# Kernel tuning notes

Measured on AMD Instinct MI355X. Metric: run time of the kernel, lower is better.

The kernel has to match this reference:

```python
import jax, jax.numpy as jnp
import numpy as np

N_NODES = 50000
N_EDGES = 800000
F_IN = 128
HIDDEN = 128
N_CLASSES = 10
N_GRAPHS = 256


def _glorot(key, shape):
    lim = float(np.sqrt(6.0 / (shape[0] + shape[1])))
    return jax.random.uniform(key, shape, jnp.float32, -lim, lim)


def setup_inputs() -> dict:
    key = jax.random.key(0)
    ks = jax.random.split(key, 12)
    x = jax.random.normal(ks[0], (N_NODES, F_IN), jnp.float32)
    edge_index = jax.random.randint(ks[1], (2, N_EDGES), 0, N_NODES, jnp.int64)
    batch = jnp.sort(jax.random.randint(ks[2], (N_NODES,), 0, N_GRAPHS, jnp.int64))
    dims = [(F_IN, HIDDEN), (HIDDEN, HIDDEN), (HIDDEN, N_CLASSES)]
    params = {}
    for i, (din, dout) in enumerate(dims, start=1):
        params[f"Wl{i}"] = _glorot(ks[2 + 2 * i], (din, dout))   # lin_l: applied to aggregated neighbors (has bias)
        params[f"bl{i}"] = jnp.zeros((dout,), jnp.float32)
        params[f"Wr{i}"] = _glorot(ks[3 + 2 * i], (din, dout))   # lin_r: applied to root/self features (no bias)
    return {"x": x, "edge_index": edge_index, "batch": batch, **params}


def _sage_conv(x, src, dst, Wl, bl, Wr):
    # mean aggregation of source features at destination nodes
    msg = x[src]                                                    # [E, D] gather
    ssum = jax.ops.segment_sum(msg, dst, num_segments=N_NODES)      # [N, D]
    cnt = jax.ops.segment_sum(jnp.ones((src.shape[0],), x.dtype), dst, num_segments=N_NODES)
    agg = ssum / jnp.maximum(cnt, 1.0)[:, None]
    return agg @ Wl + bl + x @ Wr


def reference(x, edge_index, batch, Wl1, bl1, Wr1, Wl2, bl2, Wr2, Wl3, bl3, Wr3):
    src, dst = edge_index[0], edge_index[1]
    h = _sage_conv(x, src, dst, Wl1, bl1, Wr1)
    h = _sage_conv(h, src, dst, Wl2, bl2, Wr2)
    h = _sage_conv(h, src, dst, Wl3, bl3, Wr3)                      # [N, C]
    # global mean pool over graphs
    gsum = jax.ops.segment_sum(h, batch, num_segments=N_GRAPHS)     # [G, C]
    gcnt = jax.ops.segment_sum(jnp.ones((h.shape[0],), h.dtype), batch, num_segments=N_GRAPHS)
    pooled = gsum / jnp.maximum(gcnt, 1.0)[:, None]
    return jax.nn.log_softmax(pooled, axis=-1)
```

## Files before the change

kernel.cpp:

```cpp
#include <hip/hip_runtime.h>


#define CAP 48
#define EB 4096

typedef __attribute__((ext_vector_type(8))) short short8;
typedef __attribute__((ext_vector_type(4))) float floatx4;

static __device__ __forceinline__ unsigned short f2bf(float f) {
    unsigned int u = __float_as_uint(f);
    u += 0x7FFFu + ((u >> 16) & 1u);
    return (unsigned short)(u >> 16);
}
static __device__ __forceinline__ float bf2f(unsigned short b) {
    return __uint_as_float(((unsigned int)b) << 16);
}

__global__ void prep_weights(const float* __restrict__ Wl2, const float* __restrict__ Wr2,
                             const float* __restrict__ Wl3, const float* __restrict__ Wr3,
                             float* __restrict__ m2Mg,
                             int* __restrict__ zero_base, int zero_words,
                             unsigned int* __restrict__ mmz, unsigned int* __restrict__ zb32,
                             unsigned int* __restrict__ t3b32, int N,
                             const int* __restrict__ ei, int E, int ablk, int nbk,
                             unsigned int* __restrict__ bedges, int* __restrict__ runCnt) {
    __shared__ int hist[512];
    __shared__ float wtT_s[128 * 20];
    if (blockIdx.x < (unsigned)ablk) {
        for (int i = threadIdx.x; i < nbk; i += 256) hist[i] = 0;
        __syncthreads();
        int e0 = blockIdx.x * EB + threadIdx.x;
        unsigned int pk[16];
        int bk[16], loc[16];
#pragma unroll
        for (int k = 0; k < 16; ++k) {
            int e = e0 + k * 256;
            if (e < E) {
                int src = ei[e];
                int dst = ei[E + e];
                bk[k] = dst >> 7;
                pk[k] = ((unsigned int)(dst & 127) << 16) | (unsigned int)src;
                loc[k] = atomicAdd(&hist[bk[k]], 1);
            } else bk[k] = -1;
        }
        __syncthreads();
        for (int i = threadIdx.x; i < nbk; i += 256)
            runCnt[(size_t)blockIdx.x * nbk + i] = hist[i];
#pragma unroll
        for (int k = 0; k < 16; ++k)
            if (bk[k] >= 0 && loc[k] < CAP)
                bedges[((size_t)bk[k] * ablk + blockIdx.x) * CAP + loc[k]] = pk[k];
        return;
    }
    int rb = blockIdx.x - ablk;
    if (rb < 4) {
        const int tid = threadIdx.x;
        for (int i = tid; i < 2560; i += 256) {
            int f = i / 20, c = i - f * 20;
            wtT_s[i] = (c < 10) ? Wl3[f * 10 + c] : Wr3[f * 10 + (c - 10)];
        }
        __syncthreads();
        int jl = tid >> 3;
        int cg = tid & 7;
        int j = rb * 32 + jl;
        const float* w2row = ((cg < 4) ? Wl2 : Wr2) + (size_t)j * 128;
        int c20 = (cg & 3) * 5;
        float acc[5] = {0.f, 0.f, 0.f, 0.f, 0.f};
        for (int f4 = 0; f4 < 32; ++f4) {
            float4 wv = *(const float4*)&w2row[f4 * 4];
#pragma unroll
            for (int e = 0; e < 4; ++e) {
                float w = (e == 0) ? wv.x : (e == 1) ? wv.y : (e == 2) ? wv.z : wv.w;
                const float* wt = &wtT_s[(f4 * 4 + e) * 20 + c20];
#pragma unroll
                for (int i = 0; i < 5; ++i) acc[i] += w * wt[i];
            }
        }
        int cc = (cg >> 2) * 20 + c20;
#pragma unroll
        for (int i = 0; i < 5; ++i) m2Mg[j * 40 + cc + i] = acc[i];
        return;
    }
    if (rb == 4) {
        if (threadIdx.x < 10) mmz[(size_t)N * 10 + threadIdx.x] = 0;
        if (threadIdx.x >= 32 && threadIdx.x < 42)
            zb32[(size_t)N * 10 + (threadIdx.x - 32)] = 0;
        if (threadIdx.x >= 64 && threadIdx.x < 74)
            t3b32[(size_t)N * 10 + (threadIdx.x - 64)] = 0;
        return;
    }
    int i = (rb - 5) * 256 + threadIdx.x;
    if (i < zero_words) zero_base[i] = 0;
}

__global__ __launch_bounds__(256) void prep2(
    const float* __restrict__ Wl1, const float* __restrict__ Wr1,
    const float* __restrict__ Wl3, const float* __restrict__ Wr3,
    const float* __restrict__ bl1, const float* __restrict__ bl2,
    const float* __restrict__ m2Mg, short* __restrict__ Wq,
    float* __restrict__ cbv) {
    __shared__ float m2s[128 * 40];
    __shared__ float cL[32][20];
    const int tid = threadIdx.x;
    if (blockIdx.x == 4) {
        for (int i = tid; i < 512; i += 256) {
            int k = i >> 2, f = 60 + (i & 3);
            int ks = k >> 5, rem = k & 31, qq = rem >> 3, jj = rem & 7;
            int mi = f >> 4, m = f & 15, l = qq * 16 + m;
            Wq[(((mi * 4 + ks) * 64) + l) * 8 + jj] = 0;
        }
        if (tid < 40) {
            float s = 0.f;
            if (tid < 20) {
                for (int k = 0; k < 128; ++k) s += bl1[k] * m2Mg[k * 40 + tid];
            } else {
                int c = tid - 20;
                for (int k = 0; k < 128; ++k) s += bl1[k] * m2Mg[k * 40 + 20 + c];
                for (int f = 0; f < 128; ++f) {
                    float wt = (c < 10) ? Wl3[f * 10 + c] : Wr3[f * 10 + (c - 10)];
                    s += bl2[f] * wt;
                }
            }
            cbv[tid] = s;
        }
        return;
    }
    for (int i = tid; i < 5120; i += 256) m2s[i] = m2Mg[i];
    __syncthreads();
    int kl = tid >> 3;
    int cg = tid & 7;
    int k = blockIdx.x * 32 + kl;
    int c0 = (cg & 3) * 5;
    bool left = (cg < 4);
    const float* wrow = (left ? Wl1 : Wr1) + (size_t)k * 128;
    float accM[5] = {0.f, 0.f, 0.f, 0.f, 0.f};
    float accR[5] = {0.f, 0.f, 0.f, 0.f, 0.f};
    for (int j4 = 0; j4 < 32; ++j4) {
        float4 wv = *(const float4*)&wrow[j4 * 4];
#pragma unroll
        for (int e = 0; e < 4; ++e) {
            float w = (e == 0) ? wv.x : (e == 1) ? wv.y : (e == 2) ? wv.z : wv.w;
            const float* mr = &m2s[(j4 * 4 + e) * 40];
#pragma unroll
            for (int i = 0; i < 5; ++i) {
                accM[i] += w * mr[c0 + i];
                accR[i] += w * mr[20 + c0 + i];
            }
        }
    }
    if (left) {
#pragma unroll
        for (int i = 0; i < 5; ++i) cL[kl][c0 + i] = accR[i];
    }
    __syncthreads();
    int ks = k >> 5, rem = k & 31, qq = rem >> 3, jj = rem & 7;
#pragma unroll
    for (int i = 0; i < 5; ++i) {
        if (left) {
            int f = c0 + i;
            int mi = f >> 4, m = f & 15, l = qq * 16 + m;
            Wq[(((mi * 4 + ks) * 64) + l) * 8 + jj] = (short)f2bf(accM[i]);
        } else {
            int f = 20 + c0 + i;
            int mi = f >> 4, m = f & 15, l = qq * 16 + m;
            Wq[(((mi * 4 + ks) * 64) + l) * 8 + jj] =
                (short)f2bf(accM[i] + cL[kl][c0 + i]);
            int f2 = 40 + c0 + i;
            int mi2 = f2 >> 4, m2 = f2 & 15, l2 = qq * 16 + m2;
            Wq[(((mi2 * 4 + ks) * 64) + l2) * 8 + jj] = (short)f2bf(accR[i]);
        }
    }
}

__global__ __launch_bounds__(256) void fillX(
    const float* __restrict__ x, const short* __restrict__ Wq,
    const float* __restrict__ cbv, unsigned short* __restrict__ mm,
    float* __restrict__ bmrow, int N, int nbk, int ablk,
    const unsigned int* __restrict__ bedges, const int* __restrict__ runCnt,
    int* __restrict__ cnt, unsigned short* __restrict__ colbuf) {
    __shared__ unsigned short As[64 * 136];
    __shared__ int lcnt[128];
    if (blockIdx.x >= (unsigned)nbk) {
        int blk = blockIdx.x - nbk;
        int node0 = blk * 64;
#pragma unroll
        for (int c = 0; c < 8; ++c) {
            int idx = c * 256 + threadIdx.x;
            int r = idx >> 5;
            int c4 = idx & 31;
            int row = node0 + r;
            float4 v = make_float4(0.f, 0.f, 0.f, 0.f);
            if (row < N) v = *(const float4*)&x[(size_t)row * 128 + c4 * 4];
            ushort4 p;
            p.x = f2bf(v.x); p.y = f2bf(v.y); p.z = f2bf(v.z); p.w = f2bf(v.w);
            *(ushort4*)&As[r * 136 + c4 * 4] = p;
        }
        __syncthreads();

        const int w = threadIdx.x >> 6;
        const int lane = threadIdx.x & 63;
        const int q = lane >> 4;
        const int m = lane & 15;

        floatx4 acc[4] = {};
#pragma unroll
        for (int s = 0; s < 4; ++s) {
            short8 bfrag = *(const short8*)&As[(w * 16 + m) * 136 + s * 32 + q * 8];
#pragma unroll
            for (int mi = 0; mi < 4; ++mi) {
                short8 wf = *(const short8*)&Wq[((mi * 4 + s) * 64 + lane) * 8];
                acc[mi] = __builtin_amdgcn_mfma_f32_16x16x32_bf16(
                    wf, bfrag, acc[mi], 0, 0, 0);
            }
        }
        int node = node0 + w * 16 + m;
        if (node < N) {
#pragma unroll
            for (int mi = 0; mi < 4; ++mi) {
                int f0 = mi * 16 + q * 4;
                floatx4 a = acc[mi];
                if (f0 < 20) {
                    ushort4 p;
                    p.x = f2bf(a[0]); p.y = f2bf(a[1]);
                    p.z = f2bf(a[2]); p.w = f2bf(a[3]);
                    *(ushort4*)&mm[(size_t)node * 20 + f0] = p;
                } else if (f0 < 60) {
                    float4 cb = *(const float4*)&cbv[f0 - 20];
                    float4 o = make_float4(a[0] + cb.x, a[1] + cb.y,
                                           a[2] + cb.z, a[3] + cb.w);
                    *(float4*)&bmrow[(size_t)node * 40 + (f0 - 20)] = o;
                }
            }
        }
    } else {
        int b = blockIdx.x;
        if (threadIdx.x < 128) lcnt[threadIdx.x] = 0;
        __syncthreads();
        for (int blk = threadIdx.x; blk < ablk; blk += 256) {
            int c = runCnt[(size_t)blk * nbk + b];
            c = min(c, CAP);
            size_t ebase = ((size_t)b * ablk + blk) * CAP;
            for (int i = 0; i < c; ++i) {
                unsigned int pk = bedges[ebase + i];
                int dl = pk >> 16;
                int slot = atomicAdd(&lcnt[dl], 1);
                if (slot < CAP)
                    colbuf[(size_t)(b * 128 + dl) * CAP + slot] =
                        (unsigned short)(pk & 0xFFFFu);
            }
        }
        __syncthreads();
        int node = b * 128 + threadIdx.x;
        if (threadIdx.x < 128 && node < N) cnt[node] = lcnt[threadIdx.x];
    }
}

__global__ __launch_bounds__(256) void aggM(
    const unsigned int* __restrict__ mm32, const int* __restrict__ cnt,
    const unsigned short* __restrict__ colbuf, const float2* __restrict__ bmrow2,
    unsigned int* __restrict__ zb32, int N) {
    const int lane = threadIdx.x & 63;
    const int wvi = threadIdx.x >> 6;
    const int la = lane & 15;
    const int qb = lane & 48;
    const int node = blockIdx.x * 16 + wvi * 4 + (lane >> 4);
    const bool valid = node < N;
    const int nodec = valid ? node : N - 1;
    const int deg = cnt[nodec];
    const int d = valid ? min(deg, CAP) : 0;
    const unsigned short* cb = colbuf + (size_t)nodec * CAP;

    float f0 = 0.f, f1 = 0.f;
    int nb = (d + 15) >> 4;
    for (int b = 0; b < nb; ++b) {
        int slot = b * 16 + la;
        int idx = (slot < d) ? (int)cb[slot] : N;
        unsigned int vv[16];
#pragma unroll
        for (int j = 0; j < 16; ++j) {
            int s = __shfl(idx, qb + j, 64);
            vv[j] = (la < 10) ? mm32[(size_t)s * 10 + la] : 0u;
        }
#pragma unroll
        for (int j = 0; j < 16; ++j) {
            f0 += bf2f((unsigned short)(vv[j] & 0xFFFF));
            f1 += bf2f((unsigned short)(vv[j] >> 16));
        }
    }
    if (valid && la < 10) {
        float inv = 1.0f / (float)max(deg, 1);
        float2 bp = bmrow2[(size_t)node * 20 + la];
        float v0 = f0 * inv + bp.x;
        float v1 = f1 * inv + bp.y;
        zb32[(size_t)node * 10 + la] =
            (unsigned int)f2bf(v0) | ((unsigned int)f2bf(v1) << 16);
    }
}

__global__ __launch_bounds__(256) void agg20(
    const unsigned int* __restrict__ zb32, const int* __restrict__ cnt,
    const unsigned short* __restrict__ colbuf, const float2* __restrict__ bmrow2,
    const float* __restrict__ bl3, unsigned int* __restrict__ t3b32, int N) {
    const int lane = threadIdx.x & 63;
    const int wvi = threadIdx.x >> 6;
    const int la = lane & 15;
    const int qb = lane & 48;
    const int node = blockIdx.x * 16 + wvi * 4 + (lane >> 4);
    const bool valid = node < N;
    const int nodec = valid ? node : N - 1;
    const int deg = cnt[nodec];
    const int d = valid ? min(deg, CAP) : 0;
    const unsigned short* cb = colbuf + (size_t)nodec * CAP;

    float f0 = 0.f, f1 = 0.f;
    int nb = (d + 15) >> 4;
    for (int b = 0; b < nb; ++b) {
        int slot = b * 16 + la;
        int idx = (slot < d) ? (int)cb[slot] : N;
        unsigned int vv[16];
#pragma unroll
        for (int j = 0; j < 16; ++j) {
            int s = __shfl(idx, qb + j, 64);
            vv[j] = (la < 10) ? zb32[(size_t)s * 10 + la] : 0u;
        }
#pragma unroll
        for (int j = 0; j < 16; ++j) {
            f0 += bf2f((unsigned short)(vv[j] & 0xFFFF));
            f1 += bf2f((unsigned short)(vv[j] >> 16));
        }
    }
    if (valid && la < 10) {
        float inv = 1.0f / (float)max(deg, 1);
        float2 rv = bmrow2[(size_t)node * 20 + 10 + la];
        float v0 = f0 * inv + rv.x;
        float v1 = f1 * inv + rv.y;
        if (la < 5) { v0 += bl3[2 * la]; v1 += bl3[2 * la + 1]; }
        t3b32[(size_t)node * 10 + la] =
            (unsigned int)f2bf(v0) | ((unsigned int)f2bf(v1) << 16);
    }
}

__global__ __launch_bounds__(256) void agg10_pool(
    const unsigned int* __restrict__ t3b32, const int* __restrict__ cnt,
    const unsigned short* __restrict__ colbuf, const float* __restrict__ bl3,
    const int* __restrict__ batch,
    float* __restrict__ gsum, float* __restrict__ gcnt, int N) {
    __shared__ float ls[2816];
    for (int i = threadIdx.x; i < 2816; i += 256) ls[i] = 0.f;
    __syncthreads();

    const int lane = threadIdx.x & 63;
    const int wvi = threadIdx.x >> 6;
    const int la = lane & 15;
    const int qb = lane & 48;
    const int node = blockIdx.x * 16 + wvi * 4 + (lane >> 4);
    const bool valid = node < N;
    const int nodec = valid ? node : N - 1;
    const int deg = cnt[nodec];
    const int d = valid ? min(deg, CAP) : 0;
    const unsigned short* cb = colbuf + (size_t)nodec * CAP;

    float acc0 = 0.f, acc1 = 0.f;
    int nb = (d + 15) >> 4;
    for (int b = 0; b < nb; ++b) {
        int slot = b * 16 + la;
        int idx = (slot < d) ? (int)cb[slot] : N;
        unsigned int vv[16];
#pragma unroll
        for (int j = 0; j < 16; ++j) {
            int s = __shfl(idx, qb + j, 64);
            vv[j] = (la < 5) ? t3b32[(size_t)s * 10 + la] : 0u;
        }
#pragma unroll
        for (int j = 0; j < 16; ++j) {
            acc0 += bf2f((unsigned short)(vv[j] & 0xFFFF));
            acc1 += bf2f((unsigned short)(vv[j] >> 16));
        }
    }
    if (valid && la < 5) {
        unsigned int sv = t3b32[(size_t)node * 10 + 5 + la];
        float self0 = bf2f((unsigned short)(sv & 0xFFFF));
        float self1 = bf2f((unsigned short)(sv >> 16));
        float h0 = (d > 0) ? (acc0 / (float)deg + self0) : (bl3[2 * la] + self0);
        float h1 = (d > 0) ? (acc1 / (float)deg + self1) : (bl3[2 * la + 1] + self1);
        int g = batch[node];
        atomicAdd(&ls[g * 10 + 2 * la], h0);
        atomicAdd(&ls[g * 10 + 2 * la + 1], h1);
        if (la == 0) atomicAdd(&ls[2560 + g], 1.0f);
    }
    __syncthreads();
    for (int i = threadIdx.x; i < 2816; i += 256) {
        float v = ls[i];
        if (v != 0.f) {
            if (i < 2560) atomicAdd(&gsum[i], v);
            else          atomicAdd(&gcnt[i - 2560], v);
        }
    }
}

__global__ void finalize_pool(const float* __restrict__ gsum,
                              const float* __restrict__ gcnt,
                              float* __restrict__ out, int G) {
    int g = blockIdx.x * blockDim.x + threadIdx.x;
    if (g >= G) return;
    float inv = 1.0f / fmaxf(gcnt[g], 1.0f);
    float p[10];
    float m = -1e30f;
#pragma unroll
    for (int c = 0; c < 10; ++c) { p[c] = gsum[g * 10 + c] * inv; m = fmaxf(m, p[c]); }
    float s = 0.f;
#pragma unroll
    for (int c = 0; c < 10; ++c) s += expf(p[c] - m);
    float lse = logf(s);
#pragma unroll
    for (int c = 0; c < 10; ++c) out[g * 10 + c] = p[c] - m - lse;
}

extern "C" void kernel_launch(void* const* d_in, const int* in_sizes, int n_in,
                              void* d_out, int out_size, void* d_ws, size_t ws_size,
                              hipStream_t stream) {
    const float* x    = (const float*)d_in[0];
    const int*   ei   = (const int*)d_in[1];
    const int*   batch= (const int*)d_in[2];
    const float* Wl1  = (const float*)d_in[3];
    const float* bl1  = (const float*)d_in[4];
    const float* Wr1  = (const float*)d_in[5];
    const float* Wl2  = (const float*)d_in[6];
    const float* bl2  = (const float*)d_in[7];
    const float* Wr2  = (const float*)d_in[8];
    const float* Wl3  = (const float*)d_in[9];
    const float* bl3  = (const float*)d_in[10];
    const float* Wr3  = (const float*)d_in[11];
    float* out = (float*)d_out;

    const int N = in_sizes[2];
    const int E = in_sizes[1] / 2;
    const int G = out_size / 10;
    const int ablk = (E + EB - 1) / EB;
    const int nbk  = (N + 127) >> 7;

    char* ws = (char*)d_ws;
    size_t o = 0;
    float* gsum   = (float*)(ws + o); o += (size_t)G * 10 * 4;
    float* gcnt   = (float*)(ws + o); o += (size_t)G * 4;
    size_t zero_bytes = (o + 255) & ~(size_t)255;
    o = zero_bytes;
    int*            cnt    = (int*)(ws + o);            o += (size_t)N * 4;
    unsigned short* colbuf = (unsigned short*)(ws + o); o += ((size_t)N * CAP * 2 + 255) & ~(size_t)255;
    short*          Wq     = (short*)(ws + o);          o += (size_t)8192 * 2;
    float*          cbv    = (float*)(ws + o);          o += 40 * 4;
    o = (o + 255) & ~(size_t)255;
    float*          m2Mg   = (float*)(ws + o);          o += (size_t)128 * 40 * 4;
    unsigned short* mm     = (unsigned short*)(ws + o); o += (size_t)(N + 1) * 20 * 2;
    o = (o + 255) & ~(size_t)255;
    float*          bmrow  = (float*)(ws + o);          o += (size_t)N * 40 * 4;
    unsigned short* zb     = (unsigned short*)(ws + o); o += (size_t)(N + 1) * 20 * 2;
    o = (o + 255) & ~(size_t)255;
    unsigned short* t3b    = (unsigned short*)(ws + o); o += (size_t)(N + 1) * 20 * 2;
    o = (o + 255) & ~(size_t)255;
    unsigned int*   bedges = (unsigned int*)(ws + o);   o += (size_t)nbk * ablk * CAP * 4;
    int*            runCnt = (int*)(ws + o);            o += (size_t)ablk * nbk * 4;

    int zero_words = (int)(zero_bytes / 4);
    int zblocks = (zero_words + 255) / 256;
    prep_weights<<<ablk + 5 + zblocks, 256, 0, stream>>>(
        Wl2, Wr2, Wl3, Wr3, m2Mg,
        (int*)ws, zero_words,
        (unsigned int*)mm, (unsigned int*)zb, (unsigned int*)t3b, N,
        ei, E, ablk, nbk, bedges, runCnt);

    prep2<<<5, 256, 0, stream>>>(Wl1, Wr1, Wl3, Wr3, bl1, bl2, m2Mg, Wq, cbv);

    int gblocks = (N + 63) / 64;
    int ablocks = (N + 15) / 16;
    fillX<<<nbk + gblocks, 256, 0, stream>>>(x, Wq, cbv, mm, bmrow, N,
                                             nbk, ablk, bedges, runCnt,
                                             cnt, colbuf);
    aggM<<<ablocks, 256, 0, stream>>>((const unsigned int*)mm, cnt, colbuf,
                                      (const float2*)bmrow,
                                      (unsigned int*)zb, N);
    agg20<<<ablocks, 256, 0, stream>>>((const unsigned int*)zb, cnt, colbuf,
                                       (const float2*)bmrow, bl3,
                                       (unsigned int*)t3b, N);
    agg10_pool<<<ablocks, 256, 0, stream>>>((const unsigned int*)t3b, cnt, colbuf,
                                            bl3, batch, gsum, gcnt, N);
    finalize_pool<<<1, 256, 0, stream>>>(gsum, gcnt, out, G);
}
```

Baseline: 176.0 us.

## Reformulate collapsed SAGE layers to 10-wide gathers and direct atomic CSR build

The precomputed weight products are re-factored so that every neighbor-gather stage moves 10 bf16 channels per node instead of 20. Two lanes now cover each neighbor row and their partial sums are combined with a shuffle. The two-pass bucketed CSR build (block histogram, bucket scatter, then per-bucket compaction) is replaced by a single pass of global atomics on per-node counters writing straight into colbuf. The bias folding is also reorganised. The aim is to cut gather bandwidth and remove the extra bucketing pass, at the cost of heavy global atomic contention and a nondeterministic neighbor order.

After: 198.4 us. +12.7%, slower.

```diff
diff --git a/kernel.cpp b/kernel.cpp
--- a/kernel.cpp
+++ b/kernel.cpp
@@ -15,111 +15,107 @@
 static __device__ __forceinline__ float bf2f(unsigned short b) {
     return __uint_as_float(((unsigned int)b) << 16);
 }
-
-__global__ void prep_weights(const float* __restrict__ Wl2, const float* __restrict__ Wr2,
-                             const float* __restrict__ Wl3, const float* __restrict__ Wr3,
-                             float* __restrict__ m2Mg,
-                             int* __restrict__ zero_base, int zero_words,
-                             unsigned int* __restrict__ mmz, unsigned int* __restrict__ zb32,
-                             unsigned int* __restrict__ t3b32, int N,
-                             const int* __restrict__ ei, int E, int ablk, int nbk,
-                             unsigned int* __restrict__ bedges, int* __restrict__ runCnt) {
-    __shared__ int hist[512];
+static __device__ __forceinline__ unsigned int packbf2(float a, float b) {
+    return (unsigned int)f2bf(a) | ((unsigned int)f2bf(b) << 16);
+}
+
+__global__ void prep0(int* __restrict__ cnt, int N,
+                      int* __restrict__ zero_base, int zero_words,
+                      unsigned int* __restrict__ y3z, unsigned int* __restrict__ u1z,
+                      unsigned int* __restrict__ u2w) {
+    int idx = blockIdx.x * 256 + threadIdx.x;
+    if (idx < N) { cnt[idx] = 0; return; }
+    idx -= N;
+    if (idx < zero_words) { zero_base[idx] = 0; return; }
+    idx -= zero_words;
+    if (idx < 6)  { y3z[(size_t)N * 6 + idx] = 0; return; }
+    if (idx < 12) { u1z[(size_t)N * 6 + (idx - 6)] = 0; return; }
+    if (idx < 18) { u2w[(size_t)N * 6 + (idx - 12)] = 0; return; }
+}
+
+__global__ void prep1(const int* __restrict__ ei, int E, int ablk, int N,
+                      int* __restrict__ cnt, unsigned short* __restrict__ colbuf,
+                      const float* __restrict__ Wl2, const float* __restrict__ Wr2,
+                      const float* __restrict__ Wl3, const float* __restrict__ Wr3,
+                      float* __restrict__ m2Mg) {
     __shared__ float wtT_s[128 * 20];
     if (blockIdx.x < (unsigned)ablk) {
-        for (int i = threadIdx.x; i < nbk; i += 256) hist[i] = 0;
-        __syncthreads();
         int e0 = blockIdx.x * EB + threadIdx.x;
-        unsigned int pk[16];
-        int bk[16], loc[16];
 #pragma unroll
         for (int k = 0; k < 16; ++k) {
             int e = e0 + k * 256;
             if (e < E) {
                 int src = ei[e];
                 int dst = ei[E + e];
-                bk[k] = dst >> 7;
-                pk[k] = ((unsigned int)(dst & 127) << 16) | (unsigned int)src;
-                loc[k] = atomicAdd(&hist[bk[k]], 1);
-            } else bk[k] = -1;
-        }
-        __syncthreads();
-        for (int i = threadIdx.x; i < nbk; i += 256)
-            runCnt[(size_t)blockIdx.x * nbk + i] = hist[i];
-#pragma unroll
-        for (int k = 0; k < 16; ++k)
-            if (bk[k] >= 0 && loc[k] < CAP)
-                bedges[((size_t)bk[k] * ablk + blockIdx.x) * CAP + loc[k]] = pk[k];
+                int slot = atomicAdd(&cnt[dst], 1);
+                if (slot < CAP)
+                    colbuf[(size_t)dst * CAP + slot] = (unsigned short)src;
+            }
+        }
         return;
     }
     int rb = blockIdx.x - ablk;
-    if (rb < 4) {
-        const int tid = threadIdx.x;
-        for (int i = tid; i < 2560; i += 256) {
-            int f = i / 20, c = i - f * 20;
-            wtT_s[i] = (c < 10) ? Wl3[f * 10 + c] : Wr3[f * 10 + (c - 10)];
-        }
-        __syncthreads();
-        int jl = tid >> 3;
-        int cg = tid & 7;
-        int j = rb * 32 + jl;
-        const float* w2row = ((cg < 4) ? Wl2 : Wr2) + (size_t)j * 128;
-        int c20 = (cg & 3) * 5;
-        float acc[5] = {0.f, 0.f, 0.f, 0.f, 0.f};
-        for (int f4 = 0; f4 < 32; ++f4) {
-            float4 wv = *(const float4*)&w2row[f4 * 4];
-#pragma unroll
-            for (int e = 0; e < 4; ++e) {
-                float w = (e == 0) ? wv.x : (e == 1) ? wv.y : (e == 2) ? wv.z : wv.w;
-                const float* wt = &wtT_s[(f4 * 4 + e) * 20 + c20];
-#pragma unroll
-                for (int i = 0; i < 5; ++i) acc[i] += w * wt[i];
-            }
-        }
-        int cc = (cg >> 2) * 20 + c20;
-#pragma unroll
-        for (int i = 0; i < 5; ++i) m2Mg[j * 40 + cc + i] = acc[i];
-        return;
-    }
-    if (rb == 4) {
-        if (threadIdx.x < 10) mmz[(size_t)N * 10 + threadIdx.x] = 0;
-        if (threadIdx.x >= 32 && threadIdx.x < 42)
-            zb32[(size_t)N * 10 + (threadIdx.x - 32)] = 0;
-        if (threadIdx.x >= 64 && threadIdx.x < 74)
-            t3b32[(size_t)N * 10 + (threadIdx.x - 64)] = 0;
-        return;
-    }
-    int i = (rb - 5) * 256 + threadIdx.x;
-    if (i < zero_words) zero_base[i] = 0;
+    const int tid = threadIdx.x;
+    for (int i = tid; i < 2560; i += 256) {
+        int f = i / 20, c = i - f * 20;
+        wtT_s[i] = (c < 10) ? Wl3[f * 10 + c] : Wr3[f * 10 + (c - 10)];
+    }
+    __syncthreads();
+    int jl = tid >> 3;
+    int cg = tid & 7;
+    int j = rb * 32 + jl;
+    const float* w2row = ((cg < 4) ? Wl2 : Wr2) + (size_t)j * 128;
+    int c20 = (cg & 3) * 5;
+    float acc[5] = {0.f, 0.f, 0.f, 0.f, 0.f};
+    for (int f4 = 0; f4 < 32; ++f4) {
+        float4 wv = *(const float4*)&w2row[f4 * 4];
+#pragma unroll
+        for (int e = 0; e < 4; ++e) {
+            float w = (e == 0) ? wv.x : (e == 1) ? wv.y : (e == 2) ? wv.z : wv.w;
+            const float* wt = &wtT_s[(f4 * 4 + e) * 20 + c20];
+#pragma unroll
+            for (int i = 0; i < 5; ++i) acc[i] += w * wt[i];
+        }
+    }
+    int cc = (cg >> 2) * 20 + c20;
+#pragma unroll
+    for (int i = 0; i < 5; ++i) m2Mg[j * 40 + cc + i] = acc[i];
 }
 
 __global__ __launch_bounds__(256) void prep2(
     const float* __restrict__ Wl1, const float* __restrict__ Wr1,
     const float* __restrict__ Wl3, const float* __restrict__ Wr3,
     const float* __restrict__ bl1, const float* __restrict__ bl2,
+    const float* __restrict__ bl3,
     const float* __restrict__ m2Mg, short* __restrict__ Wq,
     float* __restrict__ cbv) {
     __shared__ float m2s[128 * 40];
-    __shared__ float cL[32][20];
+    __shared__ float aLR[32][80];
     const int tid = threadIdx.x;
     if (blockIdx.x == 4) {
-        for (int i = tid; i < 512; i += 256) {
-            int k = i >> 2, f = 60 + (i & 3);
+        for (int i = tid; i < 3072; i += 256) {
+            int k = i & 127;
+            int t = i >> 7;
+            int mt = t / 6, m = 10 + t % 6;
             int ks = k >> 5, rem = k & 31, qq = rem >> 3, jj = rem & 7;
-            int mi = f >> 4, m = f & 15, l = qq * 16 + m;
-            Wq[(((mi * 4 + ks) * 64) + l) * 8 + jj] = 0;
-        }
-        if (tid < 40) {
+            int l = qq * 16 + m;
+            Wq[(((mt * 4 + ks) * 64) + l) * 8 + jj] = 0;
+        }
+        if (tid < 30) {
             float s = 0.f;
-            if (tid < 20) {
-                for (int k = 0; k < 128; ++k) s += bl1[k] * m2Mg[k * 40 + tid];
+            if (tid < 10) {
+                int c = tid;
+                for (int k = 0; k < 128; ++k) s += bl1[k] * m2Mg[k * 40 + c];
+            } else if (tid < 20) {
+                int c = tid - 10;
+                for (int k = 0; k < 128; ++k)
+                    s += bl1[k] * (m2Mg[k * 40 + 20 + c] + m2Mg[k * 40 + 10 + c]);
+                for (int f = 0; f < 128; ++f) s += bl2[f] * Wl3[f * 10 + c];
             } else {
                 int c = tid - 20;
-                for (int k = 0; k < 128; ++k) s += bl1[k] * m2Mg[k * 40 + 20 + c];
-                for (int f = 0; f < 128; ++f) {
-                    float wt = (c < 10) ? Wl3[f * 10 + c] : Wr3[f * 10 + (c - 10)];
-                    s += bl2[f] * wt;
-                }
+                for (int k = 0; k < 128; ++k) s += bl1[k] * m2Mg[k * 40 + 30 + c];
+                for (int f = 0; f < 128; ++f) s += bl2[f] * Wr3[f * 10 + c];
+                s += bl3[c];
             }
             cbv[tid] = s;
         }
@@ -130,135 +126,123 @@
     int kl = tid >> 3;
     int cg = tid & 7;
     int k = blockIdx.x * 32 + kl;
-    int c0 = (cg & 3) * 5;
-    bool left = (cg < 4);
-    const float* wrow = (left ? Wl1 : Wr1) + (size_t)k * 128;
-    float accM[5] = {0.f, 0.f, 0.f, 0.f, 0.f};
+    int c0 = cg * 5;
+    const float* wl = Wl1 + (size_t)k * 128;
+    const float* wr = Wr1 + (size_t)k * 128;
+    float accL[5] = {0.f, 0.f, 0.f, 0.f, 0.f};
     float accR[5] = {0.f, 0.f, 0.f, 0.f, 0.f};
     for (int j4 = 0; j4 < 32; ++j4) {
-        float4 wv = *(const float4*)&wrow[j4 * 4];
+        float4 wa = *(const float4*)&wl[j4 * 4];
+        float4 wb = *(const float4*)&wr[j4 * 4];
 #pragma unroll
         for (int e = 0; e < 4; ++e) {
-            float w = (e == 0) ? wv.x : (e == 1) ? wv.y : (e == 2) ? wv.z : wv.w;
-            const float* mr = &m2s[(j4 * 4 + e) * 40];
+            float wle = (e == 0) ? wa.x : (e == 1) ? wa.y : (e == 2) ? wa.z : wa.w;
+            float wre = (e == 0) ? wb.x : (e == 1) ? wb.y : (e == 2) ? wb.z : wb.w;
+            const float* mr = &m2s[(j4 * 4 + e) * 40 + c0];
 #pragma unroll
             for (int i = 0; i < 5; ++i) {
-                accM[i] += w * mr[c0 + i];
-                accR[i] += w * mr[20 + c0 + i];
+                accL[i] += wle * mr[i];
+                accR[i] += wre * mr[i];
             }
         }
     }
-    if (left) {
-#pragma unroll
-        for (int i = 0; i < 5; ++i) cL[kl][c0 + i] = accR[i];
+#pragma unroll
+    for (int i = 0; i < 5; ++i) {
+        aLR[kl][c0 + i] = accL[i];
+        aLR[kl][40 + c0 + i] = accR[i];
     }
     __syncthreads();
     int ks = k >> 5, rem = k & 31, qq = rem >> 3, jj = rem & 7;
 #pragma unroll
     for (int i = 0; i < 5; ++i) {
-        if (left) {
-            int f = c0 + i;
-            int mi = f >> 4, m = f & 15, l = qq * 16 + m;
-            Wq[(((mi * 4 + ks) * 64) + l) * 8 + jj] = (short)f2bf(accM[i]);
+        int f = c0 + i;
+        float val;
+        if (f < 10) {
+            val = aLR[kl][f];
+        } else if (f < 20) {
+            int c = f - 10;
+            val = aLR[kl][40 + c] + aLR[kl][20 + c] + aLR[kl][10 + c];
+        } else if (f < 30) {
+            int c = f - 20;
+            val = aLR[kl][40 + 10 + c] + aLR[kl][40 + 20 + c] + aLR[kl][30 + c];
         } else {
-            int f = 20 + c0 + i;
-            int mi = f >> 4, m = f & 15, l = qq * 16 + m;
-            Wq[(((mi * 4 + ks) * 64) + l) * 8 + jj] =
-                (short)f2bf(accM[i] + cL[kl][c0 + i]);
-            int f2 = 40 + c0 + i;
-            int mi2 = f2 >> 4, m2 = f2 & 15, l2 = qq * 16 + m2;
-            Wq[(((mi2 * 4 + ks) * 64) + l2) * 8 + jj] = (short)f2bf(accR[i]);
-        }
+            int c = f - 30;
+            val = aLR[kl][40 + 30 + c];
+        }
+        int mt = f / 10, c = f % 10;
+        int l = qq * 16 + c;
+        Wq[(((mt * 4 + ks) * 64) + l) * 8 + jj] = (short)f2bf(val);
     }
 }
 
 __global__ __launch_bounds__(256) void fillX(
     const float* __restrict__ x, const short* __restrict__ Wq,
-    const float* __restrict__ cbv, unsigned short* __restrict__ mm,
-    float* __restrict__ bmrow, int N, int nbk, int ablk,
-    const unsigned int* __restrict__ bedges, const int* __restrict__ runCnt,
-    int* __restrict__ cnt, unsigned short* __restrict__ colbuf) {
+    unsigned short* __restrict__ y3, float* __restrict__ yS, int N) {
     __shared__ unsigned short As[64 * 136];
-    __shared__ int lcnt[128];
-    if (blockIdx.x >= (unsigned)nbk) {
-        int blk = blockIdx.x - nbk;
-        int node0 = blk * 64;
-#pragma unroll
-        for (int c = 0; c < 8; ++c) {
-            int idx = c * 256 + threadIdx.x;
-            int r = idx >> 5;
-            int c4 = idx & 31;
-            int row = node0 + r;
-            float4 v = make_float4(0.f, 0.f, 0.f, 0.f);
-            if (row < N) v = *(const float4*)&x[(size_t)row * 128 + c4 * 4];
-            ushort4 p;
-            p.x = f2bf(v.x); p.y = f2bf(v.y); p.z = f2bf(v.z); p.w = f2bf(v.w);
-            *(ushort4*)&As[r * 136 + c4 * 4] = p;
-        }
-        __syncthreads();
-
-        const int w = threadIdx.x >> 6;
-        const int lane = threadIdx.x & 63;
-        const int q = lane >> 4;
-        const int m = lane & 15;
-
-        floatx4 acc[4] = {};
-#pragma unroll
-        for (int s = 0; s < 4; ++s) {
-            short8 bfrag = *(const short8*)&As[(w * 16 + m) * 136 + s * 32 + q * 8];
-#pragma unroll
-            for (int mi = 0; mi < 4; ++mi) {
-                short8 wf = *(const short8*)&Wq[((mi * 4 + s) * 64 + lane) * 8];
-                acc[mi] = __builtin_amdgcn_mfma_f32_16x16x32_bf16(
-                    wf, bfrag, acc[mi], 0, 0, 0);
+    int node0 = blockIdx.x * 64;
+#pragma unroll
+    for (int c = 0; c < 8; ++c) {
+        int idx = c * 256 + threadIdx.x;
+        int r = idx >> 5;
+        int c4 = idx & 31;
+        int row = node0 + r;
+        float4 v = make_float4(0.f, 0.f, 0.f, 0.f);
+        if (row < N) v = *(const float4*)&x[(size_t)row * 128 + c4 * 4];
+        ushort4 p;
+        p.x = f2bf(v.x); p.y = f2bf(v.y); p.z = f2bf(v.z); p.w = f2bf(v.w);
+        *(ushort4*)&As[r * 136 + c4 * 4] = p;
+    }
+    __syncthreads();
+
+    const int w = threadIdx.x >> 6;
+    const int lane = threadIdx.x & 63;
+    const int q = lane >> 4;
+    const int m = lane & 15;
+
+    floatx4 acc[4] = {};
+#pragma unroll
+    for (int s = 0; s < 4; ++s) {
+        short8 bfrag = *(const short8*)&As[(w * 16 + m) * 136 + s * 32 + q * 8];
+#pragma unroll
+        for (int mi = 0; mi < 4; ++mi) {
+            short8 wf = *(const short8*)&Wq[((mi * 4 + s) * 64 + lane) * 8];
+            acc[mi] = __builtin_amdgcn_mfma_f32_16x16x32_bf16(
+                wf, bfrag, acc[mi], 0, 0, 0);
+        }
+    }
+    int node = node0 + w * 16 + m;
+    if (node < N) {
+        int l = q * 4;
+        {
+            floatx4 a = acc[0];
+            if (l < 8) {
+                ushort4 p;
+                p.x = f2bf(a[0]); p.y = f2bf(a[1]);
+                p.z = f2bf(a[2]); p.w = f2bf(a[3]);
+                *(ushort4*)&y3[(size_t)node * 12 + l] = p;
+            } else if (l == 8) {
+                ushort2 p2;
+                p2.x = f2bf(a[0]); p2.y = f2bf(a[1]);
+                *(ushort2*)&y3[(size_t)node * 12 + 8] = p2;
             }
         }
-        int node = node0 + w * 16 + m;
-        if (node < N) {
-#pragma unroll
-            for (int mi = 0; mi < 4; ++mi) {
-                int f0 = mi * 16 + q * 4;
-                floatx4 a = acc[mi];
-                if (f0 < 20) {
-                    ushort4 p;
-                    p.x = f2bf(a[0]); p.y = f2bf(a[1]);
-                    p.z = f2bf(a[2]); p.w = f2bf(a[3]);
-                    *(ushort4*)&mm[(size_t)node * 20 + f0] = p;
-                } else if (f0 < 60) {
-                    float4 cb = *(const float4*)&cbv[f0 - 20];
-                    float4 o = make_float4(a[0] + cb.x, a[1] + cb.y,
-                                           a[2] + cb.z, a[3] + cb.w);
-                    *(float4*)&bmrow[(size_t)node * 40 + (f0 - 20)] = o;
-                }
+#pragma unroll
+        for (int mi = 1; mi < 4; ++mi) {
+            floatx4 a = acc[mi];
+            size_t off = (size_t)node * 36 + (mi - 1) * 12 + l;
+            if (l < 8) {
+                *(float4*)&yS[off] = make_float4(a[0], a[1], a[2], a[3]);
+            } else if (l == 8) {
+                *(float2*)&yS[off] = make_float2(a[0], a[1]);
             }
         }
-    } else {
-        int b = blockIdx.x;
-        if (threadIdx.x < 128) lcnt[threadIdx.x] = 0;
-        __syncthreads();
-        for (int blk = threadIdx.x; blk < ablk; blk += 256) {
-            int c = runCnt[(size_t)blk * nbk + b];
-            c = min(c, CAP);
-            size_t ebase = ((size_t)b * ablk + blk) * CAP;
-            for (int i = 0; i < c; ++i) {
-                unsigned int pk = bedges[ebase + i];
-                int dl = pk >> 16;
-                int slot = atomicAdd(&lcnt[dl], 1);
-                if (slot < CAP)
-                    colbuf[(size_t)(b * 128 + dl) * CAP + slot] =
-                        (unsigned short)(pk & 0xFFFFu);
-            }
-        }
-        __syncthreads();
-        int node = b * 128 + threadIdx.x;
-        if (threadIdx.x < 128 && node < N) cnt[node] = lcnt[threadIdx.x];
-    }
-}
-
-__global__ __launch_bounds__(256) void aggM(
-    const unsigned int* __restrict__ mm32, const int* __restrict__ cnt,
-    const unsigned short* __restrict__ colbuf, const float2* __restrict__ bmrow2,
-    unsigned int* __restrict__ zb32, int N) {
+    }
+}
+
+__global__ __launch_bounds__(256) void g1(
+    const unsigned int* __restrict__ y3z, const int* __restrict__ cnt,
+    const unsigned short* __restrict__ colbuf, const float2* __restrict__ yS2,
+    unsigned int* __restrict__ u1z, int N) {
     const int lane = threadIdx.x & 63;
     const int wvi = threadIdx.x >> 6;
     const int la = lane & 15;
@@ -269,38 +253,41 @@
     const int deg = cnt[nodec];
     const int d = valid ? min(deg, CAP) : 0;
     const unsigned short* cb = colbuf + (size_t)nodec * CAP;
+    const int sub = (la < 5) ? la : la - 5;
 
     float f0 = 0.f, f1 = 0.f;
     int nb = (d + 15) >> 4;
     for (int b = 0; b < nb; ++b) {
         int slot = b * 16 + la;
         int idx = (slot < d) ? (int)cb[slot] : N;
-        unsigned int vv[16];
-#pragma unroll
-        for (int j = 0; j < 16; ++j) {
-            int s = __shfl(idx, qb + j, 64);
-            vv[j] = (la < 10) ? mm32[(size_t)s * 10 + la] : 0u;
-        }
-#pragma unroll
-        for (int j = 0; j < 16; ++j) {
+        unsigned int vv[8];
+#pragma unroll
+        for (int j = 0; j < 8; ++j) {
+            int s0 = __shfl(idx, qb + 2 * j, 64);
+            int s1 = __shfl(idx, qb + 2 * j + 1, 64);
+            int sr = (la < 5) ? s0 : s1;
+            vv[j] = (la < 10) ? y3z[(size_t)sr * 6 + sub] : 0u;
+        }
+#pragma unroll
+        for (int j = 0; j < 8; ++j) {
             f0 += bf2f((unsigned short)(vv[j] & 0xFFFF));
             f1 += bf2f((unsigned short)(vv[j] >> 16));
         }
     }
-    if (valid && la < 10) {
+    int pl = (la < 5) ? (lane + 5) : (lane - 5);
+    f0 += __shfl(f0, pl, 64);
+    f1 += __shfl(f1, pl, 64);
+    if (valid && la < 5) {
         float inv = 1.0f / (float)max(deg, 1);
-        float2 bp = bmrow2[(size_t)node * 20 + la];
-        float v0 = f0 * inv + bp.x;
-        float v1 = f1 * inv + bp.y;
-        zb32[(size_t)node * 10 + la] =
-            (unsigned int)f2bf(v0) | ((unsigned int)f2bf(v1) << 16);
-    }
-}
-
-__global__ __launch_bounds__(256) void agg20(
-    const unsigned int* __restrict__ zb32, const int* __restrict__ cnt,
-    const unsigned short* __restrict__ colbuf, const float2* __restrict__ bmrow2,
-    const float* __restrict__ bl3, unsigned int* __restrict__ t3b32, int N) {
+        float2 sv = yS2[(size_t)node * 18 + la];
+        u1z[(size_t)node * 6 + la] = packbf2(f0 * inv + sv.x, f1 * inv + sv.y);
+    }
+}
+
+__global__ __launch_bounds__(256) void g2(
+    const unsigned int* __restrict__ u1z, const int* __restrict__ cnt,
+    const unsigned short* __restrict__ colbuf, const float2* __restrict__ yS2,
+    const float2* __restrict__ cbv2, unsigned int* __restrict__ u2w, int N) {
     const int lane = threadIdx.x & 63;
     const int wvi = threadIdx.x >> 6;
     const int la = lane & 15;
@@ -311,39 +298,44 @@
     const int deg = cnt[nodec];
     const int d = valid ? min(deg, CAP) : 0;
     const unsigned short* cb = colbuf + (size_t)nodec * CAP;
+    const int sub = (la < 5) ? la : la - 5;
 
     float f0 = 0.f, f1 = 0.f;
     int nb = (d + 15) >> 4;
     for (int b = 0; b < nb; ++b) {
         int slot = b * 16 + la;
         int idx = (slot < d) ? (int)cb[slot] : N;
-        unsigned int vv[16];
-#pragma unroll
-        for (int j = 0; j < 16; ++j) {
-            int s = __shfl(idx, qb + j, 64);
-            vv[j] = (la < 10) ? zb32[(size_t)s * 10 + la] : 0u;
-        }
-#pragma unroll
-        for (int j = 0; j < 16; ++j) {
+        unsigned int vv[8];
+#pragma unroll
+        for (int j = 0; j < 8; ++j) {
+            int s0 = __shfl(idx, qb + 2 * j, 64);
+            int s1 = __shfl(idx, qb + 2 * j + 1, 64);
+            int sr = (la < 5) ? s0 : s1;
+            vv[j] = (la < 10) ? u1z[(size_t)sr * 6 + sub] : 0u;
+        }
+#pragma unroll
+        for (int j = 0; j < 8; ++j) {
             f0 += bf2f((unsigned short)(vv[j] & 0xFFFF));
             f1 += bf2f((unsigned short)(vv[j] >> 16));
         }
     }
-    if (valid && la < 10) {
+    int pl = (la < 5) ? (lane + 5) : (lane - 5);
+    f0 += __shfl(f0, pl, 64);
+    f1 += __shfl(f1, pl, 64);
+    if (valid && la < 5) {
         float inv = 1.0f / (float)max(deg, 1);
-        float2 rv = bmrow2[(size_t)node * 20 + 10 + la];
-        float v0 = f0 * inv + rv.x;
-        float v1 = f1 * inv + rv.y;
-        if (la < 5) { v0 += bl3[2 * la]; v1 += bl3[2 * la + 1]; }
-        t3b32[(size_t)node * 10 + la] =
-            (unsigned int)f2bf(v0) | ((unsigned int)f2bf(v1) << 16);
-    }
-}
-
-__global__ __launch_bounds__(256) void agg10_pool(
-    const unsigned int* __restrict__ t3b32, const int* __restrict__ cnt,
-    const unsigned short* __restrict__ colbuf, const float* __restrict__ bl3,
-    const int* __restrict__ batch,
+        float2 sv = yS2[(size_t)node * 18 + 6 + la];
+        float2 v1 = cbv2[la];
+        float b0 = sv.x + ((deg > 0) ? v1.x : 0.f);
+        float b1 = sv.y + ((deg > 0) ? v1.y : 0.f);
+        u2w[(size_t)node * 6 + la] = packbf2(f0 * inv + b0, f1 * inv + b1);
+    }
+}
+
+__global__ __launch_bounds__(256) void g3pool(
+    const unsigned int* __restrict__ u2w, const int* __restrict__ cnt,
+    const unsigned short* __restrict__ colbuf, const float2* __restrict__ yS2,
+    const float2* __restrict__ cbv2, const int* __restrict__ batch,
     float* __restrict__ gsum, float* __restrict__ gcnt, int N) {
     __shared__ float ls[2816];
     for (int i = threadIdx.x; i < 2816; i += 256) ls[i] = 0.f;
@@ -359,30 +351,37 @@
     const int deg = cnt[nodec];
     const int d = valid ? min(deg, CAP) : 0;
     const unsigned short* cb = colbuf + (size_t)nodec * CAP;
-
-    float acc0 = 0.f, acc1 = 0.f;
+    const int sub = (la < 5) ? la : la - 5;
+
+    float f0 = 0.f, f1 = 0.f;
     int nb = (d + 15) >> 4;
     for (int b = 0; b < nb; ++b) {
         int slot = b * 16 + la;
         int idx = (slot < d) ? (int)cb[slot] : N;
-        unsigned int vv[16];
-#pragma unroll
-        for (int j = 0; j < 16; ++j) {
-            int s = __shfl(idx, qb + j, 64);
-            vv[j] = (la < 5) ? t3b32[(size_t)s * 10 + la] : 0u;
-        }
-#pragma unroll
-        for (int j = 0; j < 16; ++j) {
-            acc0 += bf2f((unsigned short)(vv[j] & 0xFFFF));
-            acc1 += bf2f((unsigned short)(vv[j] >> 16));
-        }
-    }
+        unsigned int vv[8];
+#pragma unroll
+        for (int j = 0; j < 8; ++j) {
+            int s0 = __shfl(idx, qb + 2 * j, 64);
+            int s1 = __shfl(idx, qb + 2 * j + 1, 64);
+            int sr = (la < 5) ? s0 : s1;
+            vv[j] = (la < 10) ? u2w[(size_t)sr * 6 + sub] : 0u;
+        }
+#pragma unroll
+        for (int j = 0; j < 8; ++j) {
+            f0 += bf2f((unsigned short)(vv[j] & 0xFFFF));
+            f1 += bf2f((unsigned short)(vv[j] >> 16));
+        }
+    }
+    int pl = (la < 5) ? (lane + 5) : (lane - 5);
+    f0 += __shfl(f0, pl, 64);
+    f1 += __shfl(f1, pl, 64);
     if (valid && la < 5) {
-        unsigned int sv = t3b32[(size_t)node * 10 + 5 + la];
-        float self0 = bf2f((unsigned short)(sv & 0xFFFF));
-        float self1 = bf2f((unsigned short)(sv >> 16));
-        float h0 = (d > 0) ? (acc0 / (float)deg + self0) : (bl3[2 * la] + self0);
-        float h1 = (d > 0) ? (acc1 / (float)deg + self1) : (bl3[2 * la + 1] + self1);
+        float inv = 1.0f / (float)max(deg, 1);
+        float2 y0 = yS2[(size_t)node * 18 + 12 + la];
+        float2 v0 = cbv2[5 + la];
+        float2 vc = cbv2[10 + la];
+        float h0 = f0 * inv + y0.x + ((deg > 0) ? v0.x : 0.f) + vc.x;
+        float h1 = f1 * inv + y0.y + ((deg > 0) ? v0.y : 0.f) + vc.y;
         int g = batch[node];
         atomicAdd(&ls[g * 10 + 2 * la], h0);
         atomicAdd(&ls[g * 10 + 2 * la + 1], h1);
@@ -437,7 +436,6 @@
     const int E = in_sizes[1] / 2;
     const int G = out_size / 10;
     const int ablk = (E + EB - 1) / EB;
-    const int nbk  = (N + 127) >> 7;
 
     char* ws = (char*)d_ws;
     size_t o = 0;
@@ -448,41 +446,41 @@
     int*            cnt    = (int*)(ws + o);            o += (size_t)N * 4;
     unsigned short* colbuf = (unsigned short*)(ws + o); o += ((size_t)N * CAP * 2 + 255) & ~(size_t)255;
     short*          Wq     = (short*)(ws + o);          o += (size_t)8192 * 2;
-    float*          cbv    = (float*)(ws + o);          o += 40 * 4;
+    float*          cbv    = (float*)(ws + o);          o += 32 * 4;
     o = (o + 255) & ~(size_t)255;
     float*          m2Mg   = (float*)(ws + o);          o += (size_t)128 * 40 * 4;
-    unsigned short* mm     = (unsigned short*)(ws + o); o += (size_t)(N + 1) * 20 * 2;
     o = (o + 255) & ~(size_t)255;
-    float*          bmrow  = (float*)(ws + o);          o += (size_t)N * 40 * 4;
-    unsigned short* zb     = (unsigned short*)(ws + o); o += (size_t)(N + 1) * 20 * 2;
+    unsigned short* y3t    = (unsigned short*)(ws + o); o += (size_t)(N + 1) * 12 * 2;
     o = (o + 255) & ~(size_t)255;
-    unsigned short* t3b    = (unsigned short*)(ws + o); o += (size_t)(N + 1) * 20 * 2;
+    float*          yS     = (float*)(ws + o);          o += (size_t)N * 36 * 4;
+    unsigned short* u1z    = (unsigned short*)(ws + o); o += (size_t)(N + 1) * 12 * 2;
     o = (o + 255) & ~(size_t)255;
-    unsigned int*   bedges = (unsigned int*)(ws + o);   o += (size_t)nbk * ablk * CAP * 4;
-    int*            runCnt = (int*)(ws + o);            o += (size_t)ablk * nbk * 4;
+    unsigned short* u2w    = (unsigned short*)(ws + o); o += (size_t)(N + 1) * 12 * 2;
+    o = (o + 255) & ~(size_t)255;
 
     int zero_words = (int)(zero_bytes / 4);
-    int zblocks = (zero_words + 255) / 256;
-    prep_weights<<<ablk + 5 + zblocks, 256, 0, stream>>>(
-        Wl2, Wr2, Wl3, Wr3, m2Mg,
-        (int*)ws, zero_words,
-        (unsigned int*)mm, (unsigned int*)zb, (unsigned int*)t3b, N,
-        ei, E, ablk, nbk, bedges, runCnt);
-
-    prep2<<<5, 256, 0, stream>>>(Wl1, Wr1, Wl3, Wr3, bl1, bl2, m2Mg, Wq, cbv);
+    int tot0 = N + zero_words + 18;
+    prep0<<<(tot0 + 255) / 256, 256, 0, stream>>>(
+        cnt, N, (int*)ws, zero_words,
+        (unsigned int*)y3t, (unsigned int*)u1z, (unsigned int*)u2w);
+
+    prep1<<<ablk + 4, 256, 0, stream>>>(ei, E, ablk, N, cnt, colbuf,
+                                        Wl2, Wr2, Wl3, Wr3, m2Mg);
+
+    prep2<<<5, 256, 0, stream>>>(Wl1, Wr1, Wl3, Wr3, bl1, bl2, bl3,
+                                 m2Mg, Wq, cbv);
 
     int gblocks = (N + 63) / 64;
     int ablocks = (N + 15) / 16;
-    fillX<<<nbk + gblocks, 256, 0, stream>>>(x, Wq, cbv, mm, bmrow, N,
-                                             nbk, ablk, bedges, runCnt,
-                                             cnt, colbuf);
-    aggM<<<ablocks, 256, 0, stream>>>((const unsigned int*)mm, cnt, colbuf,
-                                      (const float2*)bmrow,
-                                      (unsigned int*)zb, N);
-    agg20<<<ablocks, 256, 0, stream>>>((const unsigned int*)zb, cnt, colbuf,
-                                       (const float2*)bmrow, bl3,
-                                       (unsigned int*)t3b, N);
-    agg10_pool<<<ablocks, 256, 0, stream>>>((const unsigned int*)t3b, cnt, colbuf,
-                                            bl3, batch, gsum, gcnt, N);
+    fillX<<<gblocks, 256, 0, stream>>>(x, Wq, y3t, yS, N);
+
+    g1<<<ablocks, 256, 0, stream>>>((const unsigned int*)y3t, cnt, colbuf,
+                                    (const float2*)yS, (unsigned int*)u1z, N);
+    g2<<<ablocks, 256, 0, stream>>>((const unsigned int*)u1z, cnt, colbuf,
+                                    (const float2*)yS, (const float2*)cbv,
+                                    (unsigned int*)u2w, N);
+    g3pool<<<ablocks, 256, 0, stream>>>((const unsigned int*)u2w, cnt, colbuf,
+                                        (const float2*)yS, (const float2*)cbv,
+                                        batch, gsum, gcnt, N);
     finalize_pool<<<1, 256, 0, stream>>>(gsum, gcnt, out, G);
 }
```
